# Performance work log

Hardware: AMD Instinct MI355X
Metric: run time of the kernel (lower is better)

Reference implementation:

```python
import jax, jax.numpy as jnp
import numpy as np

D_MODEL = 256
NHEAD = 8
HEAD_DIM = D_MODEL // NHEAD
LN_EPS = 1e-5


def _layernorm(x, g, b):
    mu = jnp.mean(x, axis=-1, keepdims=True)
    var = jnp.mean(jnp.square(x - mu), axis=-1, keepdims=True)
    return (x - mu) * jax.lax.rsqrt(var + LN_EPS) * g + b


def setup_inputs() -> dict:
    key = jax.random.key(0)
    ks = jax.random.split(key, 12)
    N, L, S, K = 2, 4800, 4800, 64
    x = jax.random.normal(ks[0], (N, L, D_MODEL), dtype=jnp.float32)
    source = jax.random.normal(ks[1], (N, S, D_MODEL), dtype=jnp.float32)
    # precomputed epipolar-band key indices per query ([N, L, K])
    epipolar_idx = jax.random.randint(ks[2], (N, L, K), 0, S, dtype=jnp.int32)
    w = lambda k, shape: (jax.random.normal(k, shape, dtype=jnp.float32) * 0.02)
    return {
        "x": x, "source": source, "epipolar_idx": epipolar_idx,
        "Wq": w(ks[3], (D_MODEL, D_MODEL)),
        "Wk": w(ks[4], (D_MODEL, D_MODEL)),
        "Wv": w(ks[5], (D_MODEL, D_MODEL)),
        "Wm": w(ks[6], (D_MODEL, D_MODEL)),
        "W1": w(ks[7], (2 * D_MODEL, 2 * D_MODEL)),
        "W2": w(ks[8], (2 * D_MODEL, D_MODEL)),
        "g1": jnp.ones((D_MODEL,), jnp.float32),
        "b1": jnp.zeros((D_MODEL,), jnp.float32),
        "g2": jnp.ones((D_MODEL,), jnp.float32),
        "b2": jnp.zeros((D_MODEL,), jnp.float32),
    }


def reference(x, source, epipolar_idx, Wq, Wk, Wv, Wm, W1, W2, g1, b1, g2, b2):
    N, L, _ = x.shape
    q = (x @ Wq).reshape(N, L, NHEAD, HEAD_DIM)            # [N,L,H,D]
    k = (source @ Wk).reshape(N, -1, NHEAD, HEAD_DIM)      # [N,S,H,D]
    v = (source @ Wv).reshape(N, -1, NHEAD, HEAD_DIM)
    # one-to-many gather: each query attends only to its epipolar-band keys
    gather = jax.vmap(lambda t, i: t[i])                   # [N,L,K,H,D]
    kg = gather(k, epipolar_idx)
    vg = gather(v, epipolar_idx)
    scale = 1.0 / jnp.sqrt(jnp.asarray(HEAD_DIM, x.dtype))
    scores = jnp.einsum('nlhd,nlkhd->nlhk', q, kg) * scale
    attn = jax.nn.softmax(scores, axis=-1)
    msg = jnp.einsum('nlhk,nlkhd->nlhd', attn, vg).reshape(N, L, D_MODEL)
    msg = _layernorm(msg @ Wm, g1, b1)
    h = jnp.concatenate([x, msg], axis=-1) @ W1            # [N,L,2C]
    h = jax.nn.relu(h) @ W2                                # [N,L,C]
    return x + _layernorm(h, g2, b2)
```

## Files before the change

kernel.cpp:

```cpp
#include <hip/hip_runtime.h>
#include <hip/hip_bf16.h>

#define D_MODEL 256
#define LQ 4800
#define NB 2
#define MROWS (NB * LQ)
#define LN_EPS 1e-5f

typedef unsigned int u32;
typedef unsigned short u16;
typedef __attribute__((ext_vector_type(8))) short bf16x8;
typedef __attribute__((ext_vector_type(4))) float f32x4;
typedef __attribute__((ext_vector_type(2))) _Float16 f16x2;

__device__ __forceinline__ u16 f2bf(float f) {
    __hip_bfloat16 h = __float2bfloat16(f);
    return *reinterpret_cast<u16*>(&h);
}

__device__ __forceinline__ float dot2f16(u32 a, u32 b, float c) {
#if __has_builtin(__builtin_amdgcn_fdot2)
    return __builtin_amdgcn_fdot2(__builtin_bit_cast(f16x2, a),
                                  __builtin_bit_cast(f16x2, b), c, false);
#else
    f16x2 av = __builtin_bit_cast(f16x2, a), bv = __builtin_bit_cast(f16x2, b);
    c = fmaf((float)av.x, (float)bv.x, c);
    return fmaf((float)av.y, (float)bv.y, c);
#endif
}
__device__ __forceinline__ u32 pk_fma16(u32 a, u32 b, u32 c) {
    u32 d;
    asm("v_pk_fma_f16 %0, %1, %2, %3" : "=v"(d) : "v"(a), "v"(b), "v"(c));
    return d;
}
__device__ __forceinline__ u32 pk_add16(u32 a, u32 b) {
    u32 d;
    asm("v_pk_add_f16 %0, %1, %2" : "=v"(d) : "v"(a), "v"(b));
    return d;
}
__device__ __forceinline__ u32 pkrtz(float a, float b) {
    return __builtin_bit_cast(u32, __builtin_amdgcn_cvt_pkrtz(a, b));
}

__global__ __launch_bounds__(256) void prep_kernel(
    const float* __restrict__ x, const float* __restrict__ source,
    const float* __restrict__ Wq, const float* __restrict__ Wk,
    const float* __restrict__ Wv, const float* __restrict__ Wm,
    const float* __restrict__ W1, const float* __restrict__ W2,
    u16* __restrict__ xb, u16* __restrict__ sb,
    u16* __restrict__ Wqkvt, u16* __restrict__ Wmt,
    u16* __restrict__ W1t, u16* __restrict__ W2t)
{
    __shared__ float tile[16][17];
    const int t = threadIdx.x;
    int bid = blockIdx.x;

    if (bid < 4800) {
        const float* src = bid < 2400 ? x : source;
        u16* dst = bid < 2400 ? xb : sb;
        int b = bid < 2400 ? bid : bid - 2400;
        int i = (b * 256 + t) * 4;
        float4 v = *reinterpret_cast<const float4*>(src + i);
        ushort4 o; o.x = f2bf(v.x); o.y = f2bf(v.y); o.z = f2bf(v.z); o.w = f2bf(v.w);
        *reinterpret_cast<ushort4*>(dst + i) = o;
        return;
    }
    int sub = bid - 4800;
    const float* W; u16* Wt; int Nd, ldt, rowoff;
    if      (sub < 256)  { W = Wq; Wt = Wqkvt; Nd = 256; ldt = 256; rowoff = 0;   }
    else if (sub < 512)  { W = Wk; Wt = Wqkvt; Nd = 256; ldt = 256; rowoff = 256; sub -= 256; }
    else if (sub < 768)  { W = Wv; Wt = Wqkvt; Nd = 256; ldt = 256; rowoff = 512; sub -= 512; }
    else if (sub < 1024) { W = Wm; Wt = Wmt;   Nd = 256; ldt = 256; rowoff = 0;   sub -= 768; }
    else if (sub < 2048) { W = W1; Wt = W1t;   Nd = 512; ldt = 512; rowoff = 0;   sub -= 1024; }
    else                 { W = W2; Wt = W2t;   Nd = 256; ldt = 512; rowoff = 0;   sub -= 2048; }
    int ntiles = Nd >> 4;
    int tn = sub % ntiles, tk = sub / ntiles;
    int tx = t & 15, ty = t >> 4;
    tile[ty][tx] = W[(size_t)(tk * 16 + ty) * Nd + tn * 16 + tx];
    __syncthreads();
    Wt[(size_t)(rowoff + tn * 16 + ty) * ldt + tk * 16 + tx] = f2bf(tile[tx][ty]);
}

template<int BM, int BN>
__global__ __launch_bounds__(256) void gemm_mfma_kernel(
    const u16* __restrict__ A0, int lda0,
    const u16* __restrict__ A1, int lda1, int splitK, int nsel,
    const u16* __restrict__ Bt, int ldb,
    void* __restrict__ Cout,
    int M, int N, int K, int flags)
{
    __shared__ __align__(16) u16 As[BM * 32];
    __shared__ __align__(16) u16 Bs[BN * 32];

    constexpr int WM = BM / 2, WN = BN / 2;
    constexpr int FI = WM / 16, FJ = WN / 16;

    const int t  = threadIdx.x;
    const int l  = t & 63;
    const int w  = t >> 6;
    const int m0 = blockIdx.y * BM;
    const int n0 = blockIdx.x * BN;
    const int wr = w >> 1, wc = w & 1;

    if (nsel && n0 >= nsel) { A0 = A1; lda0 = lda1; }

    const int srow = l >> 2;
    const int sch  = (l & 3) ^ (srow & 3);

    f32x4 acc[FI][FJ];
#pragma unroll
    for (int i = 0; i < FI; ++i)
#pragma unroll
        for (int j = 0; j < FJ; ++j) acc[i][j] = (f32x4){0.f, 0.f, 0.f, 0.f};

    for (int k0 = 0; k0 < K; k0 += 32) {
        const u16* Ap; int kk, lda;
        if (splitK && k0 >= splitK) { Ap = A1; kk = k0 - splitK; lda = lda1; }
        else                        { Ap = A0; kk = k0;          lda = lda0; }

        if (BM >= 64) {
#pragma unroll
            for (int g = 0; g < BM / 64; ++g) {
                int grp = w * (BM / 64) + g;
                int row = grp * 16 + srow;
                const u16* asrc = Ap + (size_t)(m0 + row) * lda + kk + sch * 8;
                u32* adst = (u32*)(As + grp * 512);
                __builtin_amdgcn_global_load_lds(
                    (const __attribute__((address_space(1))) u32*)asrc,
                    (__attribute__((address_space(3))) u32*)adst, 16, 0, 0);
            }
        } else if (w < BM / 16) {
            int row = w * 16 + srow;
            const u16* asrc = Ap + (size_t)(m0 + row) * lda + kk + sch * 8;
            u32* adst = (u32*)(As + w * 512);
            __builtin_amdgcn_global_load_lds(
                (const __attribute__((address_space(1))) u32*)asrc,
                (__attribute__((address_space(3))) u32*)adst, 16, 0, 0);
        }
#pragma unroll
        for (int g = 0; g < BN / 64; ++g) {
            int grp = w * (BN / 64) + g;
            int row = grp * 16 + srow;
            const u16* bsrc = Bt + (size_t)(n0 + row) * ldb + k0 + sch * 8;
            u32* bdst = (u32*)(Bs + grp * 512);
            __builtin_amdgcn_global_load_lds(
                (const __attribute__((address_space(1))) u32*)bsrc,
                (__attribute__((address_space(3))) u32*)bdst, 16, 0, 0);
        }
        __syncthreads();

        const int r  = l & 15;
        const int ch = l >> 4;
        bf16x8 af[FI], bfr[FJ];
#pragma unroll
        for (int i = 0; i < FI; ++i) {
            int ar = wr * WM + i * 16 + r;
            af[i] = *(const bf16x8*)((const char*)As + ar * 64 + ((ch ^ (r & 3)) * 16));
        }
#pragma unroll
        for (int j = 0; j < FJ; ++j) {
            int br = wc * WN + j * 16 + r;
            bfr[j] = *(const bf16x8*)((const char*)Bs + br * 64 + ((ch ^ (r & 3)) * 16));
        }
#pragma unroll
        for (int i = 0; i < FI; ++i)
#pragma unroll
            for (int j = 0; j < FJ; ++j)
                acc[i][j] = __builtin_amdgcn_mfma_f32_16x16x32_bf16(af[i], bfr[j], acc[i][j], 0, 0, 0);
        __syncthreads();
    }

    const int r  = l & 15;
    const int q4 = l >> 4;
#pragma unroll
    for (int i = 0; i < FI; ++i)
#pragma unroll
        for (int j = 0; j < FJ; ++j) {
            int col = n0 + wc * WN + j * 16 + r;
#pragma unroll
            for (int reg = 0; reg < 4; ++reg) {
                int row = m0 + wr * WM + i * 16 + q4 * 4 + reg;
                float vv = acc[i][j][reg];
                if (flags & 1) vv = fmaxf(vv, 0.f);
                size_t off;
                int colw, Nw;
                if (flags & 4) { off = (size_t)(col >> 8) * M * 256; colw = col & 255; Nw = 256; }
                else           { off = 0; colw = col; Nw = N; }
                if (flags & 8) {
                    _Float16 hv = (_Float16)vv;
                    ((u16*)Cout)[off + (size_t)row * Nw + colw] = __builtin_bit_cast(u16, hv);
                } else if (flags & 2) {
                    ((u16*)Cout)[off + (size_t)row * Nw + colw] = f2bf(vv);
                } else {
                    ((float*)Cout)[off + (size_t)row * Nw + colw] = vv;
                }
            }
        }
}

template<int BM, bool RESID, bool OUT_BF16>
__global__ __launch_bounds__(256) void gemm_ln_kernel(
    const u16* __restrict__ A, int lda,
    const u16* __restrict__ Bt, int ldb,
    const float* __restrict__ g, const float* __restrict__ b,
    const float* __restrict__ xres,
    void* __restrict__ Cout, int K)
{
    __shared__ __align__(16) u16 As[BM * 32];
    __shared__ __align__(16) u16 Bs[256 * 32];
    __shared__ float2 red[BM][2];

    constexpr int WM = BM / 2;
    constexpr int FI = WM / 16;

    const int t  = threadIdx.x;
    const int l  = t & 63;
    const int w  = t >> 6;
    const int m0 = blockIdx.x * BM;
    const int wr = w >> 1, wc = w & 1;

    const int srow = l >> 2;
    const int sch  = (l & 3) ^ (srow & 3);

    f32x4 acc[FI][8];
#pragma unroll
    for (int i = 0; i < FI; ++i)
#pragma unroll
        for (int j = 0; j < 8; ++j) acc[i][j] = (f32x4){0.f, 0.f, 0.f, 0.f};

    for (int k0 = 0; k0 < K; k0 += 32) {
        if (w < BM / 16) {
            int row = w * 16 + srow;
            const u16* asrc = A + (size_t)(m0 + row) * lda + k0 + sch * 8;
            u32* adst = (u32*)(As + w * 512);
            __builtin_amdgcn_global_load_lds(
                (const __attribute__((address_space(1))) u32*)asrc,
                (__attribute__((address_space(3))) u32*)adst, 16, 0, 0);
        }
#pragma unroll
        for (int gg = 0; gg < 4; ++gg) {
            int grp = w * 4 + gg;
            int row = grp * 16 + srow;
            const u16* bsrc = Bt + (size_t)row * ldb + k0 + sch * 8;
            u32* bdst = (u32*)(Bs + grp * 512);
            __builtin_amdgcn_global_load_lds(
                (const __attribute__((address_space(1))) u32*)bsrc,
                (__attribute__((address_space(3))) u32*)bdst, 16, 0, 0);
        }
        __syncthreads();

        const int r  = l & 15;
        const int ch = l >> 4;
        bf16x8 af[FI], bfr[8];
#pragma unroll
        for (int i = 0; i < FI; ++i) {
            int ar = wr * WM + i * 16 + r;
            af[i] = *(const bf16x8*)((const char*)As + ar * 64 + ((ch ^ (r & 3)) * 16));
        }
#pragma unroll
        for (int j = 0; j < 8; ++j) {
            int br = wc * 128 + j * 16 + r;
            bfr[j] = *(const bf16x8*)((const char*)Bs + br * 64 + ((ch ^ (r & 3)) * 16));
        }
#pragma unroll
        for (int i = 0; i < FI; ++i)
#pragma unroll
            for (int j = 0; j < 8; ++j)
                acc[i][j] = __builtin_amdgcn_mfma_f32_16x16x32_bf16(af[i], bfr[j], acc[i][j], 0, 0, 0);
        __syncthreads();
    }

    const int r  = l & 15;
    const int q4 = l >> 4;

    float rs[FI][4], rq[FI][4];
#pragma unroll
    for (int i = 0; i < FI; ++i)
#pragma unroll
        for (int reg = 0; reg < 4; ++reg) {
            float s = 0.f, sq = 0.f;
#pragma unroll
            for (int j = 0; j < 8; ++j) {
                float vv = acc[i][j][reg];
                s += vv; sq += vv * vv;
            }
            rs[i][reg] = s; rq[i][reg] = sq;
        }
#pragma unroll
    for (int off = 1; off <= 8; off <<= 1)
#pragma unroll
        for (int i = 0; i < FI; ++i)
#pragma unroll
            for (int reg = 0; reg < 4; ++reg) {
                rs[i][reg] += __shfl_xor(rs[i][reg], off);
                rq[i][reg] += __shfl_xor(rq[i][reg], off);
            }
    if (r == 0) {
#pragma unroll
        for (int i = 0; i < FI; ++i)
#pragma unroll
            for (int reg = 0; reg < 4; ++reg) {
                int row = wr * WM + i * 16 + q4 * 4 + reg;
                red[row][wc] = make_float2(rs[i][reg], rq[i][reg]);
            }
    }
    __syncthreads();

    float gj[8], bj[8];
#pragma unroll
    for (int j = 0; j < 8; ++j) {
        int col = wc * 128 + j * 16 + r;
        gj[j] = g[col]; bj[j] = b[col];
    }

#pragma unroll
    for (int i = 0; i < FI; ++i)
#pragma unroll
        for (int reg = 0; reg < 4; ++reg) {
            int row = wr * WM + i * 16 + q4 * 4 + reg;
            float2 t0 = red[row][0], t1 = red[row][1];
            float mu  = (t0.x + t1.x) * 0.00390625f;
            float var = (t0.y + t1.y) * 0.00390625f - mu * mu;
            float rstd = rsqrtf(var + LN_EPS);
#pragma unroll
            for (int j = 0; j < 8; ++j) {
                int col = wc * 128 + j * 16 + r;
                float vv = (acc[i][j][reg] - mu) * rstd * gj[j] + bj[j];
                size_t oidx = (size_t)(m0 + row) * 256 + col;
                if (RESID) vv += xres[oidx];
                if (OUT_BF16) ((u16*)Cout)[oidx] = f2bf(vv);
                else          ((float*)Cout)[oidx] = vv;
            }
        }
}

__global__ __launch_bounds__(256, 8) void attn_kernel(
    const u16* __restrict__ q, const u16* __restrict__ k,
    const u16* __restrict__ v, const int* __restrict__ idx,
    u16* __restrict__ msg)
{
    const int t  = threadIdx.x;
    const int l  = t & 63;
    const int hp = t >> 6;
    const int qi = blockIdx.x;
    const int n  = qi / LQ;
    const size_t srcbase = (size_t)n * LQ * 256;

    const int o = l >> 3;
    const int c = l & 7;

    const int* idxp = idx + (size_t)qi * 64;
    int rows[8];
#pragma unroll
    for (int i = 0; i < 8; ++i) rows[i] = idxp[i * 8 + o];

    const size_t hoff = (size_t)hp * 64 + c * 8;

    uint4 kd[8];
#pragma unroll
    for (int i = 0; i < 8; ++i)
        kd[i] = *(const uint4*)(k + srcbase + (size_t)rows[i] * 256 + hoff);
    uint4 qc = *(const uint4*)(q + (size_t)qi * 256 + hoff);

    float s[8];
#pragma unroll
    for (int i = 0; i < 8; ++i) {
        float si = 0.f;
        si = dot2f16(kd[i].x, qc.x, si);
        si = dot2f16(kd[i].y, qc.y, si);
        si = dot2f16(kd[i].z, qc.z, si);
        si = dot2f16(kd[i].w, qc.w, si);
        si += __shfl_xor(si, 1);
        si += __shfl_xor(si, 2);
        s[i] = si * 0.17677669529663687f;
    }

    uint4 vd[8];
#pragma unroll
    for (int i = 0; i < 8; ++i)
        vd[i] = *(const uint4*)(v + srcbase + (size_t)rows[i] * 256 + hoff);

    float mx = s[0];
#pragma unroll
    for (int i = 1; i < 8; ++i) mx = fmaxf(mx, s[i]);
    mx = fmaxf(mx, __shfl_xor(mx, 8));
    mx = fmaxf(mx, __shfl_xor(mx, 16));
    mx = fmaxf(mx, __shfl_xor(mx, 32));
    float p[8], sum = 0.f;
#pragma unroll
    for (int i = 0; i < 8; ++i) { p[i] = __expf(s[i] - mx); sum += p[i]; }
    sum += __shfl_xor(sum, 8);
    sum += __shfl_xor(sum, 16);
    sum += __shfl_xor(sum, 32);
    float inv = 1.f / sum;

    u32 A0 = 0, A1 = 0, A2 = 0, A3 = 0;
#pragma unroll
    for (int i = 0; i < 8; ++i) {
        float pi = p[i] * inv;
        u32 pp = pkrtz(pi, pi);
        A0 = pk_fma16(pp, vd[i].x, A0);
        A1 = pk_fma16(pp, vd[i].y, A1);
        A2 = pk_fma16(pp, vd[i].z, A2);
        A3 = pk_fma16(pp, vd[i].w, A3);
    }

    const bool ob0 = (o & 1) != 0;
    const bool ob1 = (o & 2) != 0;
    {
        u32 t0 = ob0 ? A0 : A2;
        u32 t1 = ob0 ? A1 : A3;
        t0 = __shfl_xor((int)t0, 8);
        t1 = __shfl_xor((int)t1, 8);
        A0 = pk_add16(ob0 ? A2 : A0, t0);
        A1 = pk_add16(ob0 ? A3 : A1, t1);
    }
    {
        u32 u0 = ob1 ? A0 : A1;
        u0 = __shfl_xor((int)u0, 16);
        A0 = pk_add16(ob1 ? A1 : A0, u0);
    }
    A0 = pk_add16(A0, (u32)__shfl_xor((int)A0, 32));

    if (o < 4) {
        int j = 2 * (o & 1) + ((o >> 1) & 1);
        f16x2 hv = __builtin_bit_cast(f16x2, A0);
        u32 packed = (u32)f2bf((float)hv.x) | ((u32)f2bf((float)hv.y) << 16);
        *(u32*)(msg + (size_t)qi * 256 + hp * 64 + c * 8 + j * 2) = packed;
    }
}

extern "C" void kernel_launch(void* const* d_in, const int* in_sizes, int n_in,
                              void* d_out, int out_size, void* d_ws, size_t ws_size,
                              hipStream_t stream)
{
    const float* x      = (const float*)d_in[0];
    const float* source = (const float*)d_in[1];
    const int*   eidx   = (const int*)d_in[2];
    const float* Wq     = (const float*)d_in[3];
    const float* Wk     = (const float*)d_in[4];
    const float* Wv     = (const float*)d_in[5];
    const float* Wm     = (const float*)d_in[6];
    const float* W1     = (const float*)d_in[7];
    const float* W2     = (const float*)d_in[8];
    const float* g1     = (const float*)d_in[9];
    const float* b1     = (const float*)d_in[10];
    const float* g2     = (const float*)d_in[11];
    const float* b2     = (const float*)d_in[12];
    float* out = (float*)d_out;

    char* ws = (char*)d_ws;
    const size_t SZB = (size_t)MROWS * 256 * 2;
    u16* xb     = (u16*)(ws);
    u16* sb     = (u16*)(ws + SZB);
    u16* qb     = (u16*)(ws + 2 * SZB);
    u16* kb     = (u16*)(ws + 3 * SZB);
    u16* vb     = (u16*)(ws + 4 * SZB);
    u16* msgb   = (u16*)(ws + 5 * SZB);
    u16* msglnb = (u16*)(ws + 6 * SZB);
    u16* h1b    = (u16*)(ws + 7 * SZB);
    u16* Wqkvt  = (u16*)(ws + 9 * SZB);
    u16* Wmt    = Wqkvt + 768 * 256;
    u16* W1t    = Wmt + 256 * 256;
    u16* W2t    = W1t + 512 * 512;

    dim3 blk(256);

    prep_kernel<<<dim3(7360), blk, 0, stream>>>(x, source, Wq, Wk, Wv, Wm, W1, W2,
                                                xb, sb, Wqkvt, Wmt, W1t, W2t);

    gemm_mfma_kernel<64, 128><<<dim3(6, 150), blk, 0, stream>>>(
        xb, 256, sb, 256, 0, 256, Wqkvt, 256, qb, MROWS, 768, 256, 8 | 4);

    attn_kernel<<<dim3(MROWS), blk, 0, stream>>>(qb, kb, vb, eidx, msgb);

    gemm_ln_kernel<32, false, true><<<dim3(300), blk, 0, stream>>>(
        msgb, 256, Wmt, 256, g1, b1, nullptr, msglnb, 256);

    gemm_mfma_kernel<64, 128><<<dim3(4, 150), blk, 0, stream>>>(
        xb, 256, msglnb, 256, 256, 0, W1t, 512, h1b, MROWS, 512, 512, 1 | 2);

    gemm_ln_kernel<32, true, false><<<dim3(300), blk, 0, stream>>>(
        h1b, 512, W2t, 512, g2, b2, x, out, 512);
}
```

Before: 101.2 us.

## Fuse merge GEMM+LN, MLP W1 GEMM, and W2 GEMM+LN into one tail kernel

Replaces the three tail launches (Wm GEMM with LayerNorm, W1 GEMM with ReLU, W2 GEMM with LayerNorm and residual) with one kernel. Each block owns 32 rows and runs all three stages in sequence, writing intermediates to global memory and reading them back within the same block after a block fence and barrier. This removes two launches and keeps the intermediates hot in cache. In exchange, only 300 blocks run the W1 stage, which previously used a 600-block 64x128 tiling. The B tile in shared memory grows to 512 rows, which may lower occupancy.

```diff
diff --git a/kernel.cpp b/kernel.cpp
--- a/kernel.cpp
+++ b/kernel.cpp
@@ -40,6 +40,11 @@
 }
 __device__ __forceinline__ u32 pkrtz(float a, float b) {
     return __builtin_bit_cast(u32, __builtin_amdgcn_cvt_pkrtz(a, b));
+}
+__device__ __forceinline__ void gload_lds(const u16* src, u16* dst) {
+    __builtin_amdgcn_global_load_lds(
+        (const __attribute__((address_space(1))) u32*)src,
+        (__attribute__((address_space(3))) u32*)dst, 16, 0, 0);
 }
 
 __global__ __launch_bounds__(256) void prep_kernel(
@@ -123,29 +128,17 @@
             for (int g = 0; g < BM / 64; ++g) {
                 int grp = w * (BM / 64) + g;
                 int row = grp * 16 + srow;
-                const u16* asrc = Ap + (size_t)(m0 + row) * lda + kk + sch * 8;
-                u32* adst = (u32*)(As + grp * 512);
-                __builtin_amdgcn_global_load_lds(
-                    (const __attribute__((address_space(1))) u32*)asrc,
-                    (__attribute__((address_space(3))) u32*)adst, 16, 0, 0);
+                gload_lds(Ap + (size_t)(m0 + row) * lda + kk + sch * 8, As + grp * 512);
             }
         } else if (w < BM / 16) {
             int row = w * 16 + srow;
-            const u16* asrc = Ap + (size_t)(m0 + row) * lda + kk + sch * 8;
-            u32* adst = (u32*)(As + w * 512);
-            __builtin_amdgcn_global_load_lds(
-                (const __attribute__((address_space(1))) u32*)asrc,
-                (__attribute__((address_space(3))) u32*)adst, 16, 0, 0);
+            gload_lds(Ap + (size_t)(m0 + row) * lda + kk + sch * 8, As + w * 512);
         }
 #pragma unroll
         for (int g = 0; g < BN / 64; ++g) {
             int grp = w * (BN / 64) + g;
             int row = grp * 16 + srow;
-            const u16* bsrc = Bt + (size_t)(n0 + row) * ldb + k0 + sch * 8;
-            u32* bdst = (u32*)(Bs + grp * 512);
-            __builtin_amdgcn_global_load_lds(
-                (const __attribute__((address_space(1))) u32*)bsrc,
-                (__attribute__((address_space(3))) u32*)bdst, 16, 0, 0);
+            gload_lds(Bt + (size_t)(n0 + row) * ldb + k0 + sch * 8, Bs + grp * 512);
         }
         __syncthreads();
 
@@ -198,126 +191,97 @@
         }
 }
 
-template<int BM, bool RESID, bool OUT_BF16>
-__global__ __launch_bounds__(256) void gemm_ln_kernel(
-    const u16* __restrict__ A, int lda,
-    const u16* __restrict__ Bt, int ldb,
-    const float* __restrict__ g, const float* __restrict__ b,
-    const float* __restrict__ xres,
-    void* __restrict__ Cout, int K)
+template<int FJ>
+__device__ __forceinline__ void mm_loop(
+    const u16* __restrict__ A0, int lda0,
+    const u16* __restrict__ A1, int lda1, int splitK,
+    const u16* __restrict__ Bt, int ldb, int K, int m0,
+    u16* As, u16* Bs, f32x4 (&acc)[FJ])
 {
-    __shared__ __align__(16) u16 As[BM * 32];
-    __shared__ __align__(16) u16 Bs[256 * 32];
-    __shared__ float2 red[BM][2];
-
-    constexpr int WM = BM / 2;
-    constexpr int FI = WM / 16;
-
-    const int t  = threadIdx.x;
-    const int l  = t & 63;
-    const int w  = t >> 6;
-    const int m0 = blockIdx.x * BM;
+    const int t = threadIdx.x;
+    const int l = t & 63, w = t >> 6;
     const int wr = w >> 1, wc = w & 1;
-
     const int srow = l >> 2;
     const int sch  = (l & 3) ^ (srow & 3);
-
-    f32x4 acc[FI][8];
-#pragma unroll
-    for (int i = 0; i < FI; ++i)
-#pragma unroll
-        for (int j = 0; j < 8; ++j) acc[i][j] = (f32x4){0.f, 0.f, 0.f, 0.f};
+    const int r = l & 15, ch = l >> 4;
+
+#pragma unroll
+    for (int j = 0; j < FJ; ++j) acc[j] = (f32x4){0.f, 0.f, 0.f, 0.f};
 
     for (int k0 = 0; k0 < K; k0 += 32) {
-        if (w < BM / 16) {
+        const u16* Ap; int kk, lda;
+        if (splitK && k0 >= splitK) { Ap = A1; kk = k0 - splitK; lda = lda1; }
+        else                        { Ap = A0; kk = k0;          lda = lda0; }
+        if (w < 2) {
             int row = w * 16 + srow;
-            const u16* asrc = A + (size_t)(m0 + row) * lda + k0 + sch * 8;
-            u32* adst = (u32*)(As + w * 512);
-            __builtin_amdgcn_global_load_lds(
-                (const __attribute__((address_space(1))) u32*)asrc,
-                (__attribute__((address_space(3))) u32*)adst, 16, 0, 0);
-        }
-#pragma unroll
-        for (int gg = 0; gg < 4; ++gg) {
-            int grp = w * 4 + gg;
+            gload_lds(Ap + (size_t)(m0 + row) * lda + kk + sch * 8, As + w * 512);
+        }
+#pragma unroll
+        for (int g = 0; g < FJ / 2; ++g) {
+            int grp = w * (FJ / 2) + g;
             int row = grp * 16 + srow;
-            const u16* bsrc = Bt + (size_t)row * ldb + k0 + sch * 8;
-            u32* bdst = (u32*)(Bs + grp * 512);
-            __builtin_amdgcn_global_load_lds(
-                (const __attribute__((address_space(1))) u32*)bsrc,
-                (__attribute__((address_space(3))) u32*)bdst, 16, 0, 0);
-        }
-        __syncthreads();
-
-        const int r  = l & 15;
-        const int ch = l >> 4;
-        bf16x8 af[FI], bfr[8];
-#pragma unroll
-        for (int i = 0; i < FI; ++i) {
-            int ar = wr * WM + i * 16 + r;
-            af[i] = *(const bf16x8*)((const char*)As + ar * 64 + ((ch ^ (r & 3)) * 16));
-        }
-#pragma unroll
-        for (int j = 0; j < 8; ++j) {
-            int br = wc * 128 + j * 16 + r;
-            bfr[j] = *(const bf16x8*)((const char*)Bs + br * 64 + ((ch ^ (r & 3)) * 16));
-        }
-#pragma unroll
-        for (int i = 0; i < FI; ++i)
-#pragma unroll
-            for (int j = 0; j < 8; ++j)
-                acc[i][j] = __builtin_amdgcn_mfma_f32_16x16x32_bf16(af[i], bfr[j], acc[i][j], 0, 0, 0);
-        __syncthreads();
-    }
-
-    const int r  = l & 15;
-    const int q4 = l >> 4;
-
-    float rs[FI][4], rq[FI][4];
-#pragma unroll
-    for (int i = 0; i < FI; ++i)
+            gload_lds(Bt + (size_t)row * ldb + k0 + sch * 8, Bs + grp * 512);
+        }
+        __syncthreads();
+        bf16x8 af = *(const bf16x8*)((const char*)As + (wr * 16 + r) * 64 + ((ch ^ (r & 3)) * 16));
+#pragma unroll
+        for (int j = 0; j < FJ; ++j) {
+            int br = wc * (FJ * 16) + j * 16 + r;
+            bf16x8 bf = *(const bf16x8*)((const char*)Bs + br * 64 + ((ch ^ (r & 3)) * 16));
+            acc[j] = __builtin_amdgcn_mfma_f32_16x16x32_bf16(af, bf, acc[j], 0, 0, 0);
+        }
+        __syncthreads();
+    }
+}
+
+__global__ __launch_bounds__(256) void tail_kernel(
+    const u16* __restrict__ msg, const u16* __restrict__ xb,
+    const float* __restrict__ x,
+    const u16* __restrict__ Wmt, const u16* __restrict__ W1t,
+    const u16* __restrict__ W2t,
+    const float* __restrict__ g1, const float* __restrict__ b1,
+    const float* __restrict__ g2, const float* __restrict__ b2,
+    u16* __restrict__ msglnb, u16* __restrict__ h1b,
+    float* __restrict__ out)
+{
+    __shared__ __align__(16) u16 As[32 * 32];
+    __shared__ __align__(16) u16 Bs[512 * 32];
+    __shared__ float2 red[32][2];
+
+    const int t = threadIdx.x;
+    const int l = t & 63, w = t >> 6;
+    const int wr = w >> 1, wc = w & 1;
+    const int m0 = blockIdx.x * 32;
+    const int r = l & 15, q4 = l >> 4;
+
+    {
+        f32x4 acc[8];
+        mm_loop<8>(msg, 256, nullptr, 0, 0, Wmt, 256, 256, m0, As, Bs, acc);
+
+        float rs[4], rq[4];
 #pragma unroll
         for (int reg = 0; reg < 4; ++reg) {
             float s = 0.f, sq = 0.f;
 #pragma unroll
-            for (int j = 0; j < 8; ++j) {
-                float vv = acc[i][j][reg];
-                s += vv; sq += vv * vv;
-            }
-            rs[i][reg] = s; rq[i][reg] = sq;
-        }
-#pragma unroll
-    for (int off = 1; off <= 8; off <<= 1)
-#pragma unroll
-        for (int i = 0; i < FI; ++i)
+            for (int j = 0; j < 8; ++j) { float vv = acc[j][reg]; s += vv; sq += vv * vv; }
+            rs[reg] = s; rq[reg] = sq;
+        }
+#pragma unroll
+        for (int off = 1; off <= 8; off <<= 1)
 #pragma unroll
             for (int reg = 0; reg < 4; ++reg) {
-                rs[i][reg] += __shfl_xor(rs[i][reg], off);
-                rq[i][reg] += __shfl_xor(rq[i][reg], off);
-            }
-    if (r == 0) {
-#pragma unroll
-        for (int i = 0; i < FI; ++i)
-#pragma unroll
-            for (int reg = 0; reg < 4; ++reg) {
-                int row = wr * WM + i * 16 + q4 * 4 + reg;
-                red[row][wc] = make_float2(rs[i][reg], rq[i][reg]);
-            }
-    }
-    __syncthreads();
-
-    float gj[8], bj[8];
-#pragma unroll
-    for (int j = 0; j < 8; ++j) {
-        int col = wc * 128 + j * 16 + r;
-        gj[j] = g[col]; bj[j] = b[col];
-    }
-
-#pragma unroll
-    for (int i = 0; i < FI; ++i)
+                rs[reg] += __shfl_xor(rs[reg], off);
+                rq[reg] += __shfl_xor(rq[reg], off);
+            }
+        if (r == 0)
+#pragma unroll
+            for (int reg = 0; reg < 4; ++reg)
+                red[wr * 16 + q4 * 4 + reg][wc] = make_float2(rs[reg], rq[reg]);
+        __syncthreads();
+
 #pragma unroll
         for (int reg = 0; reg < 4; ++reg) {
-            int row = wr * WM + i * 16 + q4 * 4 + reg;
+            int row = wr * 16 + q4 * 4 + reg;
             float2 t0 = red[row][0], t1 = red[row][1];
             float mu  = (t0.x + t1.x) * 0.00390625f;
             float var = (t0.y + t1.y) * 0.00390625f - mu * mu;
@@ -325,13 +289,73 @@
 #pragma unroll
             for (int j = 0; j < 8; ++j) {
                 int col = wc * 128 + j * 16 + r;
-                float vv = (acc[i][j][reg] - mu) * rstd * gj[j] + bj[j];
+                float vv = (acc[j][reg] - mu) * rstd * g1[col] + b1[col];
+                msglnb[(size_t)(m0 + row) * 256 + col] = f2bf(vv);
+            }
+        }
+    }
+    __threadfence_block();
+    __syncthreads();
+
+    {
+        f32x4 acc[16];
+        mm_loop<16>(xb, 256, msglnb, 256, 256, W1t, 512, 512, m0, As, Bs, acc);
+#pragma unroll
+        for (int j = 0; j < 16; ++j) {
+            int col = wc * 256 + j * 16 + r;
+#pragma unroll
+            for (int reg = 0; reg < 4; ++reg) {
+                int row = wr * 16 + q4 * 4 + reg;
+                float vv = fmaxf(acc[j][reg], 0.f);
+                h1b[(size_t)(m0 + row) * 512 + col] = f2bf(vv);
+            }
+        }
+    }
+    __threadfence_block();
+    __syncthreads();
+
+    {
+        f32x4 acc[8];
+        mm_loop<8>(h1b, 512, nullptr, 0, 0, W2t, 512, 512, m0, As, Bs, acc);
+
+        float rs[4], rq[4];
+#pragma unroll
+        for (int reg = 0; reg < 4; ++reg) {
+            float s = 0.f, sq = 0.f;
+#pragma unroll
+            for (int j = 0; j < 8; ++j) { float vv = acc[j][reg]; s += vv; sq += vv * vv; }
+            rs[reg] = s; rq[reg] = sq;
+        }
+#pragma unroll
+        for (int off = 1; off <= 8; off <<= 1)
+#pragma unroll
+            for (int reg = 0; reg < 4; ++reg) {
+                rs[reg] += __shfl_xor(rs[reg], off);
+                rq[reg] += __shfl_xor(rq[reg], off);
+            }
+        __syncthreads();
+        if (r == 0)
+#pragma unroll
+            for (int reg = 0; reg < 4; ++reg)
+                red[wr * 16 + q4 * 4 + reg][wc] = make_float2(rs[reg], rq[reg]);
+        __syncthreads();
+
+#pragma unroll
+        for (int reg = 0; reg < 4; ++reg) {
+            int row = wr * 16 + q4 * 4 + reg;
+            float2 t0 = red[row][0], t1 = red[row][1];
+            float mu  = (t0.x + t1.x) * 0.00390625f;
+            float var = (t0.y + t1.y) * 0.00390625f - mu * mu;
+            float rstd = rsqrtf(var + LN_EPS);
+#pragma unroll
+            for (int j = 0; j < 8; ++j) {
+                int col = wc * 128 + j * 16 + r;
                 size_t oidx = (size_t)(m0 + row) * 256 + col;
-                if (RESID) vv += xres[oidx];
-                if (OUT_BF16) ((u16*)Cout)[oidx] = f2bf(vv);
-                else          ((float*)Cout)[oidx] = vv;
-            }
-        }
+                float vv = (acc[j][reg] - mu) * rstd * g2[col] + b2[col] + x[oidx];
+                out[oidx] = vv;
+            }
+        }
+    }
 }
 
 __global__ __launch_bounds__(256, 8) void attn_kernel(
@@ -474,12 +498,6 @@
 
     attn_kernel<<<dim3(MROWS), blk, 0, stream>>>(qb, kb, vb, eidx, msgb);
 
-    gemm_ln_kernel<32, false, true><<<dim3(300), blk, 0, stream>>>(
-        msgb, 256, Wmt, 256, g1, b1, nullptr, msglnb, 256);
-
-    gemm_mfma_kernel<64, 128><<<dim3(4, 150), blk, 0, stream>>>(
-        xb, 256, msglnb, 256, 256, 0, W1t, 512, h1b, MROWS, 512, 512, 1 | 2);
-
-    gemm_ln_kernel<32, true, false><<<dim3(300), blk, 0, stream>>>(
-        h1b, 512, W2t, 512, g2, b2, x, out, 512);
-}
+    tail_kernel<<<dim3(300), blk, 0, stream>>>(
+        msgb, xb, x, Wmt, W1t, W2t, g1, b1, g2, b2, msglnb, h1b, out);
+}
```

Result: no change. 100.1 us (-1.0%).
